# Kernel tuning notes

Hardware: AMD Instinct MI355X
Metric: run time of the kernel (lower is better)

The kernel has to match this reference:

```python
import jax, jax.numpy as jnp
import numpy as np

N = 50000   # nodes
E = 800000  # edges
D = 128     # input feature dim
H = 128     # hidden dim
L = 3       # num GIN layers
G = 64      # graphs in batch


def setup_inputs() -> dict:
    key = jax.random.key(0)
    ks = jax.random.split(key, 20)
    inp = {
        "h": jax.random.normal(ks[0], (N, D), jnp.float32),
        "src": jax.random.randint(ks[1], (E,), 0, N),
        "dst": jax.random.randint(ks[2], (E,), 0, N),
        "graph_ids": jnp.sort(jax.random.randint(ks[3], (N,), 0, G)),
    }
    k = 4
    for i in range(L):
        in_dim = D if i == 0 else H
        inp[f"w1_{i}"] = jax.random.normal(ks[k], (in_dim, H), jnp.float32) / np.sqrt(in_dim).astype(np.float32); k += 1
        inp[f"b1_{i}"] = jnp.zeros((H,), jnp.float32)
        inp[f"w2_{i}"] = jax.random.normal(ks[k], (H, H), jnp.float32) / np.sqrt(H).astype(np.float32); k += 1
        inp[f"b2_{i}"] = jnp.zeros((H,), jnp.float32)
    inp["w_out"] = jax.random.normal(ks[k], (H * L, 1), jnp.float32) / np.sqrt(H * L).astype(np.float32)
    inp["b_out"] = jnp.zeros((1,), jnp.float32)
    return inp


def _gin_layer(h, src, dst, w1, b1, w2, b2):
    # sum aggregation over edges: agg[i] = sum_{(j->i) in E} h[j]
    agg = jax.ops.segment_sum(h[src], dst, num_segments=N)
    z = h + agg  # (1 + eps) * h + agg with eps = 0 (DGL GINConv default)
    return jax.nn.relu(z @ w1 + b1) @ w2 + b2  # 2-layer MLP


def reference(h, src, dst, graph_ids,
              w1_0, b1_0, w2_0, b2_0,
              w1_1, b1_1, w2_1, b2_1,
              w1_2, b1_2, w2_2, b2_2,
              w_out, b_out):
    layers = [(w1_0, b1_0, w2_0, b2_0),
              (w1_1, b1_1, w2_1, b2_1),
              (w1_2, b1_2, w2_2, b2_2)]
    readouts = []
    for w1, b1, w2, b2 in layers:
        h = _gin_layer(h, src, dst, w1, b1, w2, b2)
        # per-graph sum readout of node features: [G, H]
        readouts.append(jax.ops.segment_sum(h, graph_ids, num_segments=G))
    hg = jnp.concatenate(readouts, axis=1)  # [G, H*L]
    return hg @ w_out + b_out  # [G, 1]
```

## Files before the change

### kernel.cpp

```cpp
#include <hip/hip_runtime.h>

#define NN 50000
#define NE 800000
#define DIMH 128
#define NGRAPH 64
#define NTILES 3125
#define PAIRS 1024
#define MLP_BLOCKS 512
#define MLP_ITERS 4
#define NBIN 196
#define BCAP 8064
#define SL_US 800000
#define SL_U4 100000

typedef __attribute__((ext_vector_type(8))) short bf16x8;
typedef __attribute__((ext_vector_type(4))) float f32x4;

__device__ __forceinline__ unsigned short f2b(float f) {
  unsigned int b = __float_as_uint(f);
  unsigned int r = (b + 0x7FFFu + ((b >> 16) & 1u)) >> 16;
  return (unsigned short)r;
}
__device__ __forceinline__ float b2f_lo(unsigned int u) { return __uint_as_float(u << 16); }
__device__ __forceinline__ float b2f_hi(unsigned int u) { return __uint_as_float(u & 0xffff0000u); }
__device__ __forceinline__ unsigned int pk2(float lo, float hi) {
  return (unsigned int)f2b(lo) | ((unsigned int)f2b(hi) << 16);
}
__device__ __forceinline__ void add8(float* a, uint4 u) {
  a[0] += b2f_lo(u.x); a[1] += b2f_hi(u.x);
  a[2] += b2f_lo(u.y); a[3] += b2f_hi(u.y);
  a[4] += b2f_lo(u.z); a[5] += b2f_hi(u.z);
  a[6] += b2f_lo(u.w); a[7] += b2f_hi(u.w);
}


__global__ __launch_bounds__(256) void bin_scatter_kernel(const int* __restrict__ src,
                                                          const int* __restrict__ dst,
                                                          int* __restrict__ gcnt,
                                                          int2* __restrict__ staging) {
  __shared__ int hist[NBIN];
  __shared__ int base[NBIN];
  int tid = threadIdx.x;
  for (int i = tid; i < NBIN; i += 256) hist[i] = 0;
  __syncthreads();
  int e0 = blockIdx.x * 2048;
  int2 ed[8];
  int bin[8], rank[8];
#pragma unroll
  for (int k = 0; k < 8; ++k) {
    int e = e0 + k * 256 + tid;
    bin[k] = 0; rank[k] = 0; ed[k] = make_int2(0, 0);
    if (e < NE) {
      ed[k].x = src[e]; ed[k].y = dst[e];
      bin[k] = ed[k].y >> 8;
      rank[k] = atomicAdd(&hist[bin[k]], 1);
    }
  }
  __syncthreads();
  for (int i = tid; i < NBIN; i += 256) base[i] = atomicAdd(&gcnt[i], hist[i]);
  __syncthreads();
#pragma unroll
  for (int k = 0; k < 8; ++k) {
    int e = e0 + k * 256 + tid;
    if (e < NE) staging[bin[k] * BCAP + base[bin[k]] + rank[k]] = ed[k];
  }
}

__global__ __launch_bounds__(256) void bin_fill_kernel(const int2* __restrict__ staging,
                                                       const int* __restrict__ gcnt,
                                                       int* __restrict__ adj,
                                                       int* __restrict__ row_ptr,
                                                       int* __restrict__ cnt,
                                                       int* __restrict__ alloc) {
  __shared__ int hdeg[256], loc[256], c2[256];
  __shared__ int sbase;
  int b = blockIdx.x;
  int tid = threadIdx.x;
  hdeg[tid] = 0; c2[tid] = 0;
  __syncthreads();
  int n = gcnt[b];
  for (int i = tid; i < n; i += 256)
    atomicAdd(&hdeg[staging[b * BCAP + i].y & 255], 1);
  __syncthreads();
  int v = hdeg[tid];
  int va = (v + 1) & ~1;
  loc[tid] = va;
  __syncthreads();
  for (int off = 1; off < 256; off <<= 1) {
    int t = (tid >= off) ? loc[tid - off] : 0;
    __syncthreads();
    loc[tid] += t;
    __syncthreads();
  }
  if (tid == 255) sbase = atomicAdd(alloc, loc[255]);
  __syncthreads();
  int excl = loc[tid] - va;
  int node = b * 256 + tid;
  if (node < NN) { row_ptr[node] = sbase + excl; cnt[node] = v; }
  loc[tid] = excl;
  __syncthreads();
  for (int i = tid; i < n; i += 256) {
    int2 e = staging[b * BCAP + i];
    int local = e.y & 255;
    int r = atomicAdd(&c2[local], 1);
    adj[sbase + loc[local] + r] = e.x;
  }
}


struct WPtrs { const float* w[6]; const float* b_out; const float* b2_last;
               const float* w_out; };

__global__ __launch_bounds__(256) void prep_kernel(WPtrs ptrs, unsigned short* __restrict__ wt,
                                                   float* __restrict__ out,
                                                   int* __restrict__ gcnt,
                                                   int* __restrict__ alloc,
                                                   float* __restrict__ v2,
                                                   float* __restrict__ s2) {
  int i = blockIdx.x * 256 + threadIdx.x;
  int m = i >> 14;
  int idx = i & 16383;
  int c = idx >> 7, k = idx & 127;
  wt[m * 16384 + idx] = f2b(ptrs.w[m][k * DIMH + c]);
  if (i < NGRAPH) out[i] = ptrs.b_out[0];
  if (i < NBIN) gcnt[i] = 0;
  if (i == NBIN) *alloc = 0;
  if (i < DIMH) {
    float s = 0.f;
    const float* w2r = ptrs.w[5] + i * DIMH;
    for (int cc = 0; cc < DIMH; ++cc) s += w2r[cc] * ptrs.w_out[2 * DIMH + cc];
    v2[i] = s;
  }
  if (i == DIMH) {
    float s = 0.f;
    for (int cc = 0; cc < DIMH; ++cc) s += ptrs.b2_last[cc] * ptrs.w_out[2 * DIMH + cc];
    *s2 = s;
  }
}

__global__ void convh_kernel(const float* __restrict__ h, uint2* __restrict__ Hs) {
  int t = blockIdx.x * 256 + threadIdx.x;
  if (t >= NN * 32) return;
  int node = t >> 5;
  int q = t & 31;
  float4 v = *(const float4*)&h[node * DIMH + q * 4];
  uint2 o;
  o.x = pk2(v.x, v.y);
  o.y = pk2(v.z, v.w);
  Hs[(q >> 2) * (SL_U4 * 2) + node * 4 + (q & 3)] = o;
}

__global__ __launch_bounds__(256) void agg_kernel(const uint4* __restrict__ Hs,
                                                  const int* __restrict__ row_ptr,
                                                  const int* __restrict__ cnt,
                                                  const int* __restrict__ adj,
                                                  uint4* __restrict__ Zs) {
  int bid = blockIdx.x;
  int slice = bid & 7;
  int nb = bid >> 3;
  int tid = threadIdx.x;
  int node = nb * 128 + (tid >> 1);
  int l2 = tid & 1;
  if (node >= NN) return;
  const uint4* hp = Hs + slice * SL_U4;
  int start = row_ptr[node];
  int c = cnt[node];
  float a[8];
  {
    uint4 own = hp[node * 2 + l2];
    a[0] = b2f_lo(own.x); a[1] = b2f_hi(own.x);
    a[2] = b2f_lo(own.y); a[3] = b2f_hi(own.y);
    a[4] = b2f_lo(own.z); a[5] = b2f_hi(own.z);
    a[6] = b2f_lo(own.w); a[7] = b2f_hi(own.w);
  }
  int j = 0;
  for (; j + 8 <= c; j += 8) {
    int2 i01 = *(const int2*)(adj + start + j);
    int2 i23 = *(const int2*)(adj + start + j + 2);
    int2 i45 = *(const int2*)(adj + start + j + 4);
    int2 i67 = *(const int2*)(adj + start + j + 6);
    uint4 u0 = hp[i01.x * 2 + l2];
    uint4 u1 = hp[i01.y * 2 + l2];
    uint4 u2 = hp[i23.x * 2 + l2];
    uint4 u3 = hp[i23.y * 2 + l2];
    uint4 u4 = hp[i45.x * 2 + l2];
    uint4 u5 = hp[i45.y * 2 + l2];
    uint4 u6 = hp[i67.x * 2 + l2];
    uint4 u7 = hp[i67.y * 2 + l2];
    add8(a, u0); add8(a, u1); add8(a, u2); add8(a, u3);
    add8(a, u4); add8(a, u5); add8(a, u6); add8(a, u7);
  }
  for (; j + 2 <= c; j += 2) {
    int2 i01 = *(const int2*)(adj + start + j);
    uint4 u0 = hp[i01.x * 2 + l2];
    uint4 u1 = hp[i01.y * 2 + l2];
    add8(a, u0); add8(a, u1);
  }
  if (j < c) {
    int n0 = adj[start + j];
    add8(a, hp[n0 * 2 + l2]);
  }
  uint4 o;
  o.x = pk2(a[0], a[1]);
  o.y = pk2(a[2], a[3]);
  o.z = pk2(a[4], a[5]);
  o.w = pk2(a[6], a[7]);
  Zs[slice * SL_U4 + node * 2 + l2] = o;
}

__global__ __launch_bounds__(256, 2) void mlp_kernel(const unsigned short* __restrict__ X,
                                                     const unsigned short* __restrict__ W1t,
                                                     const float* __restrict__ b1,
                                                     const unsigned short* __restrict__ W2t,
                                                     const float* __restrict__ b2,
                                                     unsigned short* __restrict__ Y,
                                                     const int* __restrict__ gids,
                                                     const float* __restrict__ wout,
                                                     float* __restrict__ gout,
                                                     const float* __restrict__ v2,
                                                     const float* __restrict__ s2p) {
  __shared__ unsigned short y1[2][2][2048];
  __shared__ float s_gout[NGRAPH];
  int tid = threadIdx.x;
  if (tid < NGRAPH) s_gout[tid] = 0.f;
  bool last = (v2 != nullptr);

  int wv = tid >> 6;
  int lane = tid & 63;
  int pb = wv >> 1;
  int half = wv & 1;
  int l15 = lane & 15;
  int g = lane >> 4;
  int p = blockIdx.x * 2 + pb;

  int asl_base = (g >> 1) * SL_US + (g & 1) * 8 + l15 * 16;

  bf16x8 a[4];
  {
    int roff = p * 256;
#pragma unroll
    for (int kt = 0; kt < 4; ++kt)
      a[kt] = *(const bf16x8*)(X + 2 * kt * SL_US + roff + asl_base);
  }

  bf16x8 fb1[4][4], fb2[4][4];
  const unsigned short* w1b = W1t + (half * 64 + l15) * DIMH + g * 8;
  const unsigned short* w2b = W2t + (half * 64 + l15) * DIMH + g * 8;
#pragma unroll
  for (int n = 0; n < 4; ++n)
#pragma unroll
    for (int kt = 0; kt < 4; ++kt) {
      fb1[n][kt] = *(const bf16x8*)(w1b + n * 16 * DIMH + kt * 32);
      if (!last) fb2[n][kt] = *(const bf16x8*)(w2b + n * 16 * DIMH + kt * 32);
    }
  float b1v[4], b2v[4], wov[4], v2v[4];
  float s2v = last ? *s2p : 0.f;
#pragma unroll
  for (int n = 0; n < 4; ++n) {
    int col = half * 64 + n * 16 + l15;
    b1v[n] = b1[col];
    b2v[n] = last ? 0.f : b2[col];
    wov[n] = last ? 0.f : wout[col];
    v2v[n] = last ? v2[col] : 0.f;
  }
  __syncthreads();

#pragma unroll
  for (int i = 0; i < MLP_ITERS; ++i) {
    int rtc = p + i * PAIRS;
    bool active = rtc < NTILES;
    unsigned short* buf = y1[pb][i & 1];

    if (active) {
      float pr1[4] = {0.f, 0.f, 0.f, 0.f};
#pragma unroll
      for (int n = 0; n < 4; ++n) {
        f32x4 acc = (f32x4){0.f, 0.f, 0.f, 0.f};
#pragma unroll
        for (int kt = 0; kt < 4; ++kt)
          acc = __builtin_amdgcn_mfma_f32_16x16x32_bf16(a[kt], fb1[n][kt], acc, 0, 0, 0);
        int col2 = (half * 64 + n * 16 + l15) * 2;
#pragma unroll
        for (int r = 0; r < 4; ++r) {
          float f = fmaxf(acc[r] + b1v[n], 0.f);
          if (!last) {
            int row = 4 * g + r;
            buf[((row * 256 + col2) ^ (row << 4)) >> 1] = f2b(f);
          } else {
            pr1[r] += f * v2v[n];
          }
        }
      }
      if (last) {
#pragma unroll
        for (int r = 0; r < 4; ++r) {
#pragma unroll
          for (int off = 1; off < 16; off <<= 1) pr1[r] += __shfl_xor(pr1[r], off, 64);
        }
        if (l15 == 0) {
          float s2add = (half == 0) ? s2v : 0.f;
#pragma unroll
          for (int r = 0; r < 4; ++r)
            atomicAdd(&s_gout[gids[rtc * 16 + 4 * g + r]], pr1[r] + s2add);
        }
      }
    }

    int rtn = p + (i + 1) * PAIRS;
    if (i + 1 < MLP_ITERS && rtn < NTILES) {
      int roff = rtn * 256;
#pragma unroll
      for (int kt = 0; kt < 4; ++kt)
        a[kt] = *(const bf16x8*)(X + 2 * kt * SL_US + roff + asl_base);
    }

    __syncthreads();

    if (active && !last) {
      bf16x8 a2[4];
#pragma unroll
      for (int kt = 0; kt < 4; ++kt)
        a2[kt] = *(const bf16x8*)&buf[((l15 * 256 + kt * 64 + g * 16) ^ (l15 << 4)) >> 1];

      float pr[4] = {0.f, 0.f, 0.f, 0.f};
#pragma unroll
      for (int n = 0; n < 4; ++n) {
        f32x4 acc = (f32x4){0.f, 0.f, 0.f, 0.f};
#pragma unroll
        for (int kt = 0; kt < 4; ++kt)
          acc = __builtin_amdgcn_mfma_f32_16x16x32_bf16(a2[kt], fb2[n][kt], acc, 0, 0, 0);
        int sl = 4 * half + n;
#pragma unroll
        for (int r = 0; r < 4; ++r) {
          float f = acc[r] + b2v[n];
          Y[sl * SL_US + (rtc * 16 + 4 * g + r) * 16 + l15] = f2b(f);
          pr[r] += f * wov[n];
        }
      }
#pragma unroll
      for (int r = 0; r < 4; ++r) {
#pragma unroll
        for (int off = 1; off < 16; off <<= 1) pr[r] += __shfl_xor(pr[r], off, 64);
      }
      if (l15 == 0) {
#pragma unroll
        for (int r = 0; r < 4; ++r)
          atomicAdd(&s_gout[gids[rtc * 16 + 4 * g + r]], pr[r]);
      }
    }
  }

  __syncthreads();
  if (tid < NGRAPH) {
    float v = s_gout[tid];
    if (v != 0.f) atomicAdd(&gout[tid], v);
  }
}


extern "C" void kernel_launch(void* const* d_in, const int* in_sizes, int n_in,
                              void* d_out, int out_size, void* d_ws, size_t ws_size,
                              hipStream_t stream) {
  const float* h = (const float*)d_in[0];
  const int* src = (const int*)d_in[1];
  const int* dst = (const int*)d_in[2];
  const int* gids = (const int*)d_in[3];
  const float* w_out = (const float*)d_in[16];
  const float* b_out = (const float*)d_in[17];
  float* out = (float*)d_out;

  char* base = (char*)d_ws;
  unsigned short* buf0 = (unsigned short*)(base);
  unsigned short* buf1 = (unsigned short*)(base + 12800000);
  int2* staging = (int2*)(base + 25600000);
  int* adj = (int*)(base + 38400000);
  int* row_ptr = (int*)(base + 41800064);
  int* cnt = (int*)(base + 42000128);
  int* gcnt = (int*)(base + 42200192);
  int* alloc = (int*)(base + 42201024);
  unsigned short* wt = (unsigned short*)(base + 42201088);
  float* v2 = (float*)(base + 42397696);
  float* s2 = (float*)(base + 42398208);
  unsigned short* Zs = (unsigned short*)(base + 42400000);

  WPtrs ptrs;
  for (int l = 0; l < 3; ++l) {
    ptrs.w[2 * l] = (const float*)d_in[4 + l * 4];
    ptrs.w[2 * l + 1] = (const float*)d_in[6 + l * 4];
  }
  ptrs.b_out = b_out;
  ptrs.b2_last = (const float*)d_in[15];
  ptrs.w_out = w_out;

  prep_kernel<<<384, 256, 0, stream>>>(ptrs, wt, out, gcnt, alloc, v2, s2);
  bin_scatter_kernel<<<(NE + 2047) / 2048, 256, 0, stream>>>(src, dst, gcnt, staging);
  bin_fill_kernel<<<NBIN, 256, 0, stream>>>(staging, gcnt, adj, row_ptr, cnt, alloc);
  convh_kernel<<<(NN * 32 + 255) / 256, 256, 0, stream>>>(h, (uint2*)buf0);

  int agg_blocks = 391 * 8;

  for (int l = 0; l < 3; ++l) {
    const float* b1 = (const float*)d_in[5 + l * 4];
    const float* b2 = (const float*)d_in[7 + l * 4];
    const unsigned short* Hl = (l & 1) ? buf1 : buf0;
    unsigned short* Yl = (l & 1) ? buf0 : buf1;
    int lastl = (l == 2);
    agg_kernel<<<agg_blocks, 256, 0, stream>>>((const uint4*)Hl, row_ptr, cnt, adj,
                                               (uint4*)Zs);
    mlp_kernel<<<MLP_BLOCKS, 256, 0, stream>>>(Zs, wt + (2 * l) * 16384, b1,
                                               wt + (2 * l + 1) * 16384, b2,
                                               lastl ? nullptr : Yl,
                                               gids, w_out + l * DIMH, out,
                                               lastl ? v2 : nullptr,
                                               lastl ? s2 : nullptr);
  }
}
```

Baseline: 220.6 us.

## Give each MLP block a single tile pair and defer W2 fragment loads

The MLP kernel no longer loops four times over persistent tile pairs. It now launches one block per tile pair (1563 blocks) and raises the launch-bounds occupancy hint from 2 to 4. W2 fragments and the bias and output weights are loaded only after the first GEMM, which shrinks live registers and halves the shared y1 buffer so more waves can fit per CU. The change gives up the software prefetch of the next tile's activations and reloads weights in every block, leaning on occupancy to hide latency instead; the prep kernel's dot products are also split into four accumulators.

```diff
diff --git a/kernel.cpp b/kernel.cpp
--- a/kernel.cpp
+++ b/kernel.cpp
@@ -5,9 +5,7 @@
 #define DIMH 128
 #define NGRAPH 64
 #define NTILES 3125
-#define PAIRS 1024
-#define MLP_BLOCKS 512
-#define MLP_ITERS 4
+#define MLP_BLOCKS 1563
 #define NBIN 196
 #define BCAP 8064
 #define SL_US 800000
@@ -126,15 +124,29 @@
   if (i < NBIN) gcnt[i] = 0;
   if (i == NBIN) *alloc = 0;
   if (i < DIMH) {
-    float s = 0.f;
     const float* w2r = ptrs.w[5] + i * DIMH;
-    for (int cc = 0; cc < DIMH; ++cc) s += w2r[cc] * ptrs.w_out[2 * DIMH + cc];
-    v2[i] = s;
+    const float* wo = ptrs.w_out + 2 * DIMH;
+    float s0 = 0.f, s1 = 0.f, sa = 0.f, sb = 0.f;
+#pragma unroll 4
+    for (int cc = 0; cc < DIMH; cc += 4) {
+      s0 += w2r[cc] * wo[cc];
+      s1 += w2r[cc + 1] * wo[cc + 1];
+      sa += w2r[cc + 2] * wo[cc + 2];
+      sb += w2r[cc + 3] * wo[cc + 3];
+    }
+    v2[i] = (s0 + s1) + (sa + sb);
   }
   if (i == DIMH) {
-    float s = 0.f;
-    for (int cc = 0; cc < DIMH; ++cc) s += ptrs.b2_last[cc] * ptrs.w_out[2 * DIMH + cc];
-    *s2 = s;
+    const float* wo = ptrs.w_out + 2 * DIMH;
+    float s0 = 0.f, s1 = 0.f, sa = 0.f, sb = 0.f;
+#pragma unroll 4
+    for (int cc = 0; cc < DIMH; cc += 4) {
+      s0 += ptrs.b2_last[cc] * wo[cc];
+      s1 += ptrs.b2_last[cc + 1] * wo[cc + 1];
+      sa += ptrs.b2_last[cc + 2] * wo[cc + 2];
+      sb += ptrs.b2_last[cc + 3] * wo[cc + 3];
+    }
+    *s2 = (s0 + s1) + (sa + sb);
   }
 }
 
@@ -208,7 +220,7 @@
   Zs[slice * SL_U4 + node * 2 + l2] = o;
 }
 
-__global__ __launch_bounds__(256, 2) void mlp_kernel(const unsigned short* __restrict__ X,
+__global__ __launch_bounds__(256, 4) void mlp_kernel(const unsigned short* __restrict__ X,
                                                      const unsigned short* __restrict__ W1t,
                                                      const float* __restrict__ b1,
                                                      const unsigned short* __restrict__ W2t,
@@ -219,7 +231,7 @@
                                                      float* __restrict__ gout,
                                                      const float* __restrict__ v2,
                                                      const float* __restrict__ s2p) {
-  __shared__ unsigned short y1[2][2][2048];
+  __shared__ unsigned short y1[2][2048];
   __shared__ float s_gout[NGRAPH];
   int tid = threadIdx.x;
   if (tid < NGRAPH) s_gout[tid] = 0.f;
@@ -231,92 +243,92 @@
   int half = wv & 1;
   int l15 = lane & 15;
   int g = lane >> 4;
-  int p = blockIdx.x * 2 + pb;
+  int rtc = blockIdx.x * 2 + pb;
+  bool active = rtc < NTILES;
+  int rts = active ? rtc : 0;
 
   int asl_base = (g >> 1) * SL_US + (g & 1) * 8 + l15 * 16;
-
   bf16x8 a[4];
   {
-    int roff = p * 256;
+    int roff = rts * 256;
 #pragma unroll
     for (int kt = 0; kt < 4; ++kt)
       a[kt] = *(const bf16x8*)(X + 2 * kt * SL_US + roff + asl_base);
   }
 
-  bf16x8 fb1[4][4], fb2[4][4];
+  bf16x8 fb1[4][4];
   const unsigned short* w1b = W1t + (half * 64 + l15) * DIMH + g * 8;
-  const unsigned short* w2b = W2t + (half * 64 + l15) * DIMH + g * 8;
 #pragma unroll
   for (int n = 0; n < 4; ++n)
 #pragma unroll
-    for (int kt = 0; kt < 4; ++kt) {
+    for (int kt = 0; kt < 4; ++kt)
       fb1[n][kt] = *(const bf16x8*)(w1b + n * 16 * DIMH + kt * 32);
-      if (!last) fb2[n][kt] = *(const bf16x8*)(w2b + n * 16 * DIMH + kt * 32);
-    }
-  float b1v[4], b2v[4], wov[4], v2v[4];
-  float s2v = last ? *s2p : 0.f;
+
+  float b1v[4], v2v[4];
 #pragma unroll
   for (int n = 0; n < 4; ++n) {
     int col = half * 64 + n * 16 + l15;
     b1v[n] = b1[col];
-    b2v[n] = last ? 0.f : b2[col];
-    wov[n] = last ? 0.f : wout[col];
     v2v[n] = last ? v2[col] : 0.f;
   }
-  __syncthreads();
-
-#pragma unroll
-  for (int i = 0; i < MLP_ITERS; ++i) {
-    int rtc = p + i * PAIRS;
-    bool active = rtc < NTILES;
-    unsigned short* buf = y1[pb][i & 1];
+  float s2v = last ? *s2p : 0.f;
+  __syncthreads();
+
+  unsigned short* buf = y1[pb];
+  if (active) {
+    float pr1[4] = {0.f, 0.f, 0.f, 0.f};
+#pragma unroll
+    for (int n = 0; n < 4; ++n) {
+      f32x4 acc = (f32x4){0.f, 0.f, 0.f, 0.f};
+#pragma unroll
+      for (int kt = 0; kt < 4; ++kt)
+        acc = __builtin_amdgcn_mfma_f32_16x16x32_bf16(a[kt], fb1[n][kt], acc, 0, 0, 0);
+      int col2 = (half * 64 + n * 16 + l15) * 2;
+#pragma unroll
+      for (int r = 0; r < 4; ++r) {
+        float f = fmaxf(acc[r] + b1v[n], 0.f);
+        if (!last) {
+          int row = 4 * g + r;
+          buf[((row * 256 + col2) ^ (row << 4)) >> 1] = f2b(f);
+        } else {
+          pr1[r] += f * v2v[n];
+        }
+      }
+    }
+    if (last) {
+#pragma unroll
+      for (int r = 0; r < 4; ++r) {
+#pragma unroll
+        for (int off = 1; off < 16; off <<= 1) pr1[r] += __shfl_xor(pr1[r], off, 64);
+      }
+      if (l15 == 0) {
+        float s2add = (half == 0) ? s2v : 0.f;
+#pragma unroll
+        for (int r = 0; r < 4; ++r)
+          atomicAdd(&s_gout[gids[rtc * 16 + 4 * g + r]], pr1[r] + s2add);
+      }
+    }
+  }
+
+  if (!last) {
+    bf16x8 fb2[4][4];
+    const unsigned short* w2b = W2t + (half * 64 + l15) * DIMH + g * 8;
+#pragma unroll
+    for (int n = 0; n < 4; ++n)
+#pragma unroll
+      for (int kt = 0; kt < 4; ++kt)
+        fb2[n][kt] = *(const bf16x8*)(w2b + n * 16 * DIMH + kt * 32);
+    float b2v[4], wov[4];
+#pragma unroll
+    for (int n = 0; n < 4; ++n) {
+      int col = half * 64 + n * 16 + l15;
+      b2v[n] = b2[col];
+      wov[n] = wout[col];
+    }
+
+    __syncthreads();
 
     if (active) {
-      float pr1[4] = {0.f, 0.f, 0.f, 0.f};
-#pragma unroll
-      for (int n = 0; n < 4; ++n) {
-        f32x4 acc = (f32x4){0.f, 0.f, 0.f, 0.f};
-#pragma unroll
-        for (int kt = 0; kt < 4; ++kt)
-          acc = __builtin_amdgcn_mfma_f32_16x16x32_bf16(a[kt], fb1[n][kt], acc, 0, 0, 0);
-        int col2 = (half * 64 + n * 16 + l15) * 2;
-#pragma unroll
-        for (int r = 0; r < 4; ++r) {
-          float f = fmaxf(acc[r] + b1v[n], 0.f);
-          if (!last) {
-            int row = 4 * g + r;
-            buf[((row * 256 + col2) ^ (row << 4)) >> 1] = f2b(f);
-          } else {
-            pr1[r] += f * v2v[n];
-          }
-        }
-      }
-      if (last) {
-#pragma unroll
-        for (int r = 0; r < 4; ++r) {
-#pragma unroll
-          for (int off = 1; off < 16; off <<= 1) pr1[r] += __shfl_xor(pr1[r], off, 64);
-        }
-        if (l15 == 0) {
-          float s2add = (half == 0) ? s2v : 0.f;
-#pragma unroll
-          for (int r = 0; r < 4; ++r)
-            atomicAdd(&s_gout[gids[rtc * 16 + 4 * g + r]], pr1[r] + s2add);
-        }
-      }
-    }
-
-    int rtn = p + (i + 1) * PAIRS;
-    if (i + 1 < MLP_ITERS && rtn < NTILES) {
-      int roff = rtn * 256;
-#pragma unroll
-      for (int kt = 0; kt < 4; ++kt)
-        a[kt] = *(const bf16x8*)(X + 2 * kt * SL_US + roff + asl_base);
-    }
-
-    __syncthreads();
-
-    if (active && !last) {
       bf16x8 a2[4];
 #pragma unroll
       for (int kt = 0; kt < 4; ++kt)
```

Result: slower. 237.0 us (+7.4%).
